# Kernel tuning notes

Measured on AMD Instinct MI355X. Metric: run time of the kernel, lower is better.

The kernel has to match this reference:

```python
import jax, jax.numpy as jnp
import numpy as np

B, H, W, C = 16, 64, 64, 256
NH = 8          # num_heads
WS = 8          # window size (8,8) from shift=2
HID = 1024      # mlp hidden = 4*C
EPS = 1e-5


def _rel_index():
    # relative_position_index exactly as in the torch module (meshgrid 'ij')
    ch = np.arange(WS)
    coords = np.stack(np.meshgrid(ch, ch, indexing='ij'))          # (2, WS, WS)
    flat = coords.reshape(2, -1)                                    # (2, N)
    rel = flat[:, :, None] - flat[:, None, :]                       # (2, N, N)
    rel = rel.transpose(1, 2, 0).astype(np.int64)                   # (N, N, 2)
    rel[..., 0] += WS - 1
    rel[..., 1] += WS - 1
    rel[..., 0] *= 2 * WS - 1
    return jnp.asarray(rel.sum(-1))                                 # (N, N)


def _ln(x, w, b):
    m = x.mean(-1, keepdims=True)
    v = jnp.mean((x - m) ** 2, axis=-1, keepdims=True)
    return (x - m) / jnp.sqrt(v + EPS) * w + b


def setup_inputs() -> dict:
    key = jax.random.key(0)
    ks = jax.random.split(key, 16)
    std = 0.02
    n_bias = (2 * WS - 1) * (2 * WS - 1)  # 225
    return {
        'x': jax.random.normal(ks[0], (B, H * W, C), jnp.float32),
        'norm1_w': jnp.ones((C,), jnp.float32),
        'norm1_b': jnp.zeros((C,), jnp.float32),
        'qkv_w': jax.random.normal(ks[1], (3 * C, C), jnp.float32) * std,
        'qkv_b': jnp.zeros((3 * C,), jnp.float32),
        'rel_bias': jax.random.normal(ks[2], (n_bias, NH), jnp.float32) * std,
        'proj_w': jax.random.normal(ks[3], (C, C), jnp.float32) * std,
        'proj_b': jnp.zeros((C,), jnp.float32),
        'norm2_w': jnp.ones((C,), jnp.float32),
        'norm2_b': jnp.zeros((C,), jnp.float32),
        'fc1_w': jax.random.normal(ks[4], (HID, C), jnp.float32) * std,
        'fc1_b': jnp.zeros((HID,), jnp.float32),
        'dw_w': jax.random.normal(ks[5], (3, 3, 1, HID), jnp.float32) * std,  # HWIO depthwise
        'dw_b': jnp.zeros((HID,), jnp.float32),
        'fc2_w': jax.random.normal(ks[6], (C, HID), jnp.float32) * std,
        'fc2_b': jnp.zeros((C,), jnp.float32),
    }


def reference(x, norm1_w, norm1_b, qkv_w, qkv_b, rel_bias, proj_w, proj_b,
              norm2_w, norm2_b, fc1_w, fc1_b, dw_w, dw_b, fc2_w, fc2_b):
    S = (H // WS) * (W // WS)   # num windows = 64
    N = WS * WS                 # tokens per window = 64
    shortcut = x
    h = _ln(x, norm1_w, norm1_b).reshape(B, H, W, C)
    # window partition -> (B, S, N, C), then permute to (B, N, S, C)
    hw = (h.reshape(B, H // WS, WS, W // WS, WS, C)
            .transpose(0, 1, 3, 2, 4, 5)
            .reshape(B, S, N, C))
    xw = hw.transpose(0, 2, 1, 3)            # (B, N, S, C)
    # qkv over flattened (N*S) tokens; heads split the S*C feature dim
    xf = xw.reshape(B, N * S, C)
    qkv = xf @ qkv_w.T + qkv_b               # (B, N*S, 3C)
    qkv = qkv.reshape(B, N, 3, NH, S * C // NH).transpose(2, 0, 3, 1, 4)
    q, k, v = qkv[0], qkv[1], qkv[2]         # (B, NH, N, S*C/NH)
    scale = (C // NH) ** -0.5
    attn = jnp.einsum('bhnd,bhmd->bhnm', q, k) * scale   # (B, NH, N, N)
    idx = _rel_index()
    bias = rel_bias[idx.reshape(-1)].reshape(N, N, NH).transpose(2, 0, 1)
    attn = jax.nn.softmax(attn + bias[None], axis=-1)
    out = jnp.einsum('bhnm,bhmd->bhnd', attn, v)         # (B, NH, N, S*C/NH)
    out = out.transpose(0, 2, 1, 3).reshape(B, N * S, C)
    out = (out @ proj_w.T + proj_b).reshape(B, N, S, C).transpose(0, 2, 1, 3)  # (B,S,N,C)
    # window reverse -> (B, H*W, C)
    xr = (out.reshape(B, H // WS, W // WS, WS, WS, C)
             .transpose(0, 1, 3, 2, 4, 5)
             .reshape(B, H * W, C))
    x = shortcut + xr
    # conv-based MLP (eval mode, dropout = identity)
    y = _ln(x, norm2_w, norm2_b).reshape(B, H, H, C)      # NHWC
    y = jnp.einsum('bhwc,oc->bhwo', y, fc1_w) + fc1_b     # 1x1 conv
    y = jax.lax.conv_general_dilated(
        y, dw_w, (1, 1), 'SAME',
        dimension_numbers=('NHWC', 'HWIO', 'NHWC'),
        feature_group_count=HID) + dw_b
    y = jax.nn.gelu(y, approximate=False)
    y = jnp.einsum('bhwo,co->bhwc', y, fc2_w) + fc2_b     # 1x1 conv
    return x + y.reshape(B, H * W, C)
```

## Files before the change

### kernel.cpp

```cpp
#include <hip/hip_runtime.h>
#include <hip/hip_bf16.h>
#include <cstdint>
#include <cstddef>

#define B_     16
#define HW_    4096
#define C_     256
#define NH_    8
#define S_     64
#define N_     64
#define C3_    768
#define HID_   1024
#define DHEAD_ 2048
#define EPS_   1e-5f

using u16 = unsigned short;
using u32 = unsigned int;

typedef __attribute__((ext_vector_type(8))) short bf16x8;
typedef __attribute__((ext_vector_type(4))) float f32x4;

__device__ __forceinline__ float bf2f(u16 u) {
  union { float f; u32 i; } x; x.i = ((u32)u) << 16; return x.f;
}
__device__ __forceinline__ u16 f2bf(float f) {
  union { float f; u32 i; } x; x.f = f;
  u32 r = (x.i + 0x7FFFu + ((x.i >> 16) & 1u)) >> 16;
  return (u16)r;
}

__device__ __forceinline__ void gload_lds16(const u16* g, u16* l) {
  __builtin_amdgcn_global_load_lds(
      (const __attribute__((address_space(1))) unsigned int*)g,
      (__attribute__((address_space(3))) unsigned int*)l, 16, 0, 0);
}

__launch_bounds__(256)
__global__ void f2bf_kernel(const float* __restrict__ in, u16* __restrict__ out) {
  int i = blockIdx.x * 256 + threadIdx.x;
  float4 v = ((const float4*)in)[i];
  ushort4 o = {f2bf(v.x), f2bf(v.y), f2bf(v.z), f2bf(v.w)};
  ((ushort4*)out)[i] = o;
}

__launch_bounds__(256)
__global__ void ln_kernel(const float* __restrict__ in, const float* __restrict__ w,
                          const float* __restrict__ bias, u16* __restrict__ out,
                          int b_base) {
  int wave = threadIdx.x >> 6;
  int lane = threadIdx.x & 63;
  int t = blockIdx.x * 4 + wave;
  int b = b_base + (t >> 12);
  int r = t & 4095;
  int n = r >> 6, s = r & 63;
  int hw = (((s >> 3) << 3) + (n >> 3)) * 64 + ((s & 7) << 3) + (n & 7);
  size_t src_row = ((size_t)b << 12) + hw;
  float4 v = ((const float4*)(in + src_row * C_))[lane];
  float sum = v.x + v.y + v.z + v.w;
#pragma unroll
  for (int off = 32; off; off >>= 1) sum += __shfl_xor(sum, off);
  float mean = sum * (1.0f / C_);
  float4 d = {v.x - mean, v.y - mean, v.z - mean, v.w - mean};
  float ss = d.x * d.x + d.y * d.y + d.z * d.z + d.w * d.w;
#pragma unroll
  for (int off = 32; off; off >>= 1) ss += __shfl_xor(ss, off);
  float rstd = rsqrtf(ss * (1.0f / C_) + EPS_);
  float4 w4 = ((const float4*)w)[lane];
  float4 b4 = ((const float4*)bias)[lane];
  ushort4 o;
  o.x = f2bf(d.x * rstd * w4.x + b4.x);
  o.y = f2bf(d.y * rstd * w4.y + b4.y);
  o.z = f2bf(d.z * rstd * w4.z + b4.z);
  o.w = f2bf(d.w * rstd * w4.w + b4.w);
  ((ushort4*)(out + (size_t)t * C_))[lane] = o;
}

template<int K_, int J_, int EPI>
__launch_bounds__(256)
__global__ void gemm_mfma(const u16* __restrict__ A, const u16* __restrict__ Wb,
                          const float* __restrict__ bias, u16* __restrict__ outB,
                          float* __restrict__ outF, const float* __restrict__ res,
                          int m_base, u16* __restrict__ qb, u16* __restrict__ kb,
                          u16* __restrict__ vt) {
  __shared__ u16 As[128 * 32];
  __shared__ u16 Bs[128 * 32];
  int tid = threadIdx.x;
  int wid = tid >> 6, lane = tid & 63;
  int n0 = blockIdx.x * 128;
  int m0 = blockIdx.y * 128;
  int wr = wid >> 1, wc = wid & 1;
  f32x4 acc[4][4] = {};

  int srow = lane >> 2;
  int scol = (lane & 3) * 8;

  for (int k0 = 0; k0 < K_; k0 += 32) {
#pragma unroll
    for (int r = 0; r < 2; ++r) {
      const u16* ga = A + (size_t)(m0 + r * 64 + wid * 16 + srow) * K_ + k0 + scol;
      gload_lds16(ga, &As[r * 2048 + wid * 512]);
      const u16* gb = Wb + (size_t)(n0 + r * 64 + wid * 16 + srow) * K_ + k0 + scol;
      gload_lds16(gb, &Bs[r * 2048 + wid * 512]);
    }
    __syncthreads();
    bf16x8 afr[4], bfr[4];
#pragma unroll
    for (int mf = 0; mf < 4; ++mf)
      afr[mf] = *(const bf16x8*)&As[(wr * 64 + mf * 16 + (lane & 15)) * 32 + (lane >> 4) * 8];
#pragma unroll
    for (int nf = 0; nf < 4; ++nf)
      bfr[nf] = *(const bf16x8*)&Bs[(wc * 64 + nf * 16 + (lane & 15)) * 32 + (lane >> 4) * 8];
#pragma unroll
    for (int mf = 0; mf < 4; ++mf)
#pragma unroll
      for (int nf = 0; nf < 4; ++nf)
        acc[mf][nf] = __builtin_amdgcn_mfma_f32_16x16x32_bf16(afr[mf], bfr[nf], acc[mf][nf], 0, 0, 0);
    __syncthreads();
  }

#pragma unroll
  for (int nf = 0; nf < 4; ++nf) {
    int col = n0 + wc * 64 + nf * 16 + (lane & 15);
    float bv = bias[col];
#pragma unroll
    for (int mf = 0; mf < 4; ++mf) {
#pragma unroll
      for (int j = 0; j < 4; ++j) {
        int m = m0 + wr * 64 + mf * 16 + (lane >> 4) * 4 + j;
        float v = acc[mf][nf][j] + bv;
        if (EPI == 0) {
          outB[(size_t)m * J_ + col] = f2bf(v);
        } else if (EPI == 2) {
          size_t o = (size_t)(m_base + m) * C_ + col;
          outF[o] += v;
        } else {
          int b_rel = m >> 12, nn = (m >> 6) & 63, s = m & 63;
          int f = s * 768 + col;
          int part = f >> 14, hh = (f >> 11) & 7, d = f & 2047;
          u16 val = f2bf(v);
          size_t bh = (size_t)b_rel * 8 + hh;
          if (part == 0)      qb[(bh * 64 + nn) * 2048 + d] = val;
          else if (part == 1) kb[(bh * 64 + nn) * 2048 + d] = val;
          else                vt[(bh * 2048 + d) * 64 + nn] = val;
        }
      }
    }
  }
}

__launch_bounds__(256)
__global__ void proj_ln_fused(const u16* __restrict__ A, const u16* __restrict__ Wb,
                              const float* __restrict__ bias, const float* __restrict__ res,
                              float* __restrict__ outF, const float* __restrict__ ln_w,
                              const float* __restrict__ ln_b, u16* __restrict__ h2,
                              int m_base) {
  __shared__ u16 As[64 * 32];
  __shared__ u16 Bs[256 * 32];
  __shared__ float red[64][8];
  int tid = threadIdx.x;
  int wid = tid >> 6, lane = tid & 63;
  int m0 = blockIdx.x * 64;
  f32x4 acc[4][4] = {};
  int srow = lane >> 2, scol = (lane & 3) * 8;

  for (int k0 = 0; k0 < 256; k0 += 32) {
    gload_lds16(A + (size_t)(m0 + wid * 16 + srow) * 256 + k0 + scol, &As[wid * 512]);
#pragma unroll
    for (int r = 0; r < 4; ++r)
      gload_lds16(Wb + (size_t)(r * 64 + wid * 16 + srow) * 256 + k0 + scol,
                  &Bs[(r * 64 + wid * 16) * 32]);
    __syncthreads();
    bf16x8 afr[4], bfr[4];
#pragma unroll
    for (int mf = 0; mf < 4; ++mf)
      afr[mf] = *(const bf16x8*)&As[(mf * 16 + (lane & 15)) * 32 + (lane >> 4) * 8];
#pragma unroll
    for (int nf = 0; nf < 4; ++nf)
      bfr[nf] = *(const bf16x8*)&Bs[(wid * 64 + nf * 16 + (lane & 15)) * 32 + (lane >> 4) * 8];
#pragma unroll
    for (int mf = 0; mf < 4; ++mf)
#pragma unroll
      for (int nf = 0; nf < 4; ++nf)
        acc[mf][nf] = __builtin_amdgcn_mfma_f32_16x16x32_bf16(afr[mf], bfr[nf], acc[mf][nf], 0, 0, 0);
    __syncthreads();
  }

#pragma unroll
  for (int mf = 0; mf < 4; ++mf) {
#pragma unroll
    for (int j = 0; j < 4; ++j) {
      int m = m0 + mf * 16 + (lane >> 4) * 4 + j;
      int gm = m_base + m;
      int b = gm >> 12, nn = (gm >> 6) & 63, s = gm & 63;
      int hw = (((s >> 3) << 3) + (nn >> 3)) * 64 + ((s & 7) << 3) + (nn & 7);
      size_t rowo = (((size_t)b << 12) + hw) * C_;
      float s1 = 0.f, s2 = 0.f;
#pragma unroll
      for (int nf = 0; nf < 4; ++nf) {
        int col = wid * 64 + nf * 16 + (lane & 15);
        float v = acc[mf][nf][j] + bias[col] + res[rowo + col];
        acc[mf][nf][j] = v;
        outF[rowo + col] = v;
        s1 += v; s2 += v * v;
      }
#pragma unroll
      for (int off = 1; off < 16; off <<= 1) {
        s1 += __shfl_xor(s1, off);
        s2 += __shfl_xor(s2, off);
      }
      if ((lane & 15) == 0) {
        int rr = mf * 16 + (lane >> 4) * 4 + j;
        red[rr][wid * 2] = s1;
        red[rr][wid * 2 + 1] = s2;
      }
    }
  }
  __syncthreads();

#pragma unroll
  for (int mf = 0; mf < 4; ++mf) {
#pragma unroll
    for (int j = 0; j < 4; ++j) {
      int rr = mf * 16 + (lane >> 4) * 4 + j;
      float sum = red[rr][0] + red[rr][2] + red[rr][4] + red[rr][6];
      float ssq = red[rr][1] + red[rr][3] + red[rr][5] + red[rr][7];
      float mean = sum * (1.0f / C_);
      float var = ssq * (1.0f / C_) - mean * mean;
      float rstd = rsqrtf(var + EPS_);
      int m = m0 + rr;
      int b_rel = m >> 12, nn = (m >> 6) & 63, s = m & 63;
      int hw = (((s >> 3) << 3) + (nn >> 3)) * 64 + ((s & 7) << 3) + (nn & 7);
      size_t ho = (((size_t)b_rel << 12) + hw) * C_;
#pragma unroll
      for (int nf = 0; nf < 4; ++nf) {
        int col = wid * 64 + nf * 16 + (lane & 15);
        float nv = (acc[mf][nf][j] - mean) * rstd * ln_w[col] + ln_b[col];
        h2[ho + col] = f2bf(nv);
      }
    }
  }
}

__launch_bounds__(256)
__global__ void attn_mfma(const u16* __restrict__ qb, const u16* __restrict__ kb,
                          const u16* __restrict__ vt, const float* __restrict__ rel_bias,
                          u16* __restrict__ outp) {
  __shared__ u16 bufA[4096];
  __shared__ u16 bufB[4096];
  int bh = blockIdx.x;
  int h = bh & 7;
  int b_rel = bh >> 3;
  int tid = threadIdx.x;
  int w = tid >> 6, lane = tid & 63;
  int l3 = lane >> 3, l7 = lane & 7;
  const u16* qg = qb + (size_t)bh * 64 * 2048;
  const u16* kg = kb + (size_t)bh * 64 * 2048;
  const u16* vg = vt + (size_t)bh * 2048 * 64;

  f32x4 acc[4] = {};
  for (int k0 = 0; k0 < 2048; k0 += 64) {
#pragma unroll
    for (int r = 0; r < 2; ++r) {
      int row = w * 16 + r * 8 + l3;
      int sc = (l7 ^ (row & 7)) * 8;
      gload_lds16(qg + (size_t)row * 2048 + k0 + sc, &bufA[(w * 16 + r * 8) * 64]);
      gload_lds16(kg + (size_t)row * 2048 + k0 + sc, &bufB[(w * 16 + r * 8) * 64]);
    }
    __syncthreads();
    int rowq = w * 16 + (lane & 15);
#pragma unroll
    for (int ks = 0; ks < 2; ++ks) {
      bf16x8 aq = *(const bf16x8*)&bufA[rowq * 64 + (((ks * 4 + (lane >> 4)) ^ (rowq & 7)) << 3)];
#pragma unroll
      for (int cf = 0; cf < 4; ++cf) {
        int m = cf * 16 + (lane & 15);
        bf16x8 bk = *(const bf16x8*)&bufB[m * 64 + (((ks * 4 + (lane >> 4)) ^ (m & 7)) << 3)];
        acc[cf] = __builtin_amdgcn_mfma_f32_16x16x32_bf16(aq, bk, acc[cf], 0, 0, 0);
      }
    }
    __syncthreads();
  }

  const float scale = 0.17677669529663688f;
#pragma unroll
  for (int j = 0; j < 4; ++j) {
    int r = w * 16 + (lane >> 4) * 4 + j;
    int i1 = r >> 3, j1 = r & 7;
    float v[4];
#pragma unroll
    for (int cf = 0; cf < 4; ++cf) {
      int c = cf * 16 + (lane & 15);
      int idx = (i1 - (c >> 3) + 7) * 15 + (j1 - (c & 7) + 7);
      v[cf] = acc[cf][j] * scale + rel_bias[idx * NH_ + h];
    }
    float mx = fmaxf(fmaxf(v[0], v[1]), fmaxf(v[2], v[3]));
#pragma unroll
    for (int off = 8; off; off >>= 1) mx = fmaxf(mx, __shfl_xor(mx, off));
    float sm = 0.f;
#pragma unroll
    for (int cf = 0; cf < 4; ++cf) { v[cf] = __expf(v[cf] - mx); sm += v[cf]; }
#pragma unroll
    for (int off = 8; off; off >>= 1) sm += __shfl_xor(sm, off);
    float inv = 1.0f / sm;
#pragma unroll
    for (int cf = 0; cf < 4; ++cf) {
      int c = cf * 16 + (lane & 15);
      bufA[r * 64 + (c ^ ((r & 7) << 3))] = f2bf(v[cf] * inv);
    }
  }
  __syncthreads();

  bf16x8 pa[2];
  {
    int n = w * 16 + (lane & 15);
#pragma unroll
    for (int ks = 0; ks < 2; ++ks)
      pa[ks] = *(const bf16x8*)&bufA[n * 64 + ((ks * 32 + (lane >> 4) * 8) ^ ((n & 7) << 3))];
  }

  for (int d0 = 0; d0 < 2048; d0 += 64) {
#pragma unroll
    for (int r = 0; r < 2; ++r) {
      int drow = w * 16 + r * 8 + l3;
      int sc = (l7 ^ (drow & 7)) * 8;
      gload_lds16(vg + (size_t)(d0 + drow) * 64 + sc, &bufB[(w * 16 + r * 8) * 64]);
    }
    __syncthreads();
    f32x4 o[4] = {};
#pragma unroll
    for (int ks = 0; ks < 2; ++ks)
#pragma unroll
      for (int cf = 0; cf < 4; ++cf) {
        int d = cf * 16 + (lane & 15);
        bf16x8 bv = *(const bf16x8*)&bufB[d * 64 + (((ks * 4 + (lane >> 4)) ^ (d & 7)) << 3)];
        o[cf] = __builtin_amdgcn_mfma_f32_16x16x32_bf16(pa[ks], bv, o[cf], 0, 0, 0);
      }
#pragma unroll
    for (int cf = 0; cf < 4; ++cf) {
      int f = h * 2048 + d0 + cf * 16 + (lane & 15);
      int s = f >> 8, c = f & 255;
#pragma unroll
      for (int j = 0; j < 4; ++j) {
        int n = w * 16 + (lane >> 4) * 4 + j;
        outp[(((size_t)b_rel * 64 + n) * 64 + s) * 256 + c] = f2bf(o[cf][j]);
      }
    }
    __syncthreads();
  }
}

__launch_bounds__(256)
__global__ void dwconv_gelu(const u16* __restrict__ y1, const float* __restrict__ dw_w,
                            const float* __restrict__ dw_b, u16* __restrict__ y2) {
  int bid = blockIdx.x;
  int wt = bid & 31, ht = (bid >> 5) & 15, b = bid >> 9;
  int h0 = ht * 4, w0 = wt * 2;
  int c0 = threadIdx.x * 4;

  float4 wv[9];
#pragma unroll
  for (int i = 0; i < 9; ++i) wv[i] = *(const float4*)&dw_w[i * HID_ + c0];

  ushort4 in[6][4];
#pragma unroll
  for (int ii = 0; ii < 6; ++ii) {
    int hh = h0 + ii - 1;
#pragma unroll
    for (int jj = 0; jj < 4; ++jj) {
      int ww = w0 + jj - 1;
      if ((unsigned)hh < 64u && (unsigned)ww < 64u)
        in[ii][jj] = *(const ushort4*)(y1 + ((size_t)((b << 12) + hh * 64 + ww)) * HID_ + c0);
      else
        in[ii][jj] = ushort4{0, 0, 0, 0};
    }
  }

  float4 bv = *(const float4*)&dw_b[c0];
  float4 acc[4][2];
#pragma unroll
  for (int i = 0; i < 4; ++i)
#pragma unroll
    for (int j = 0; j < 2; ++j) acc[i][j] = bv;

#pragma unroll
  for (int ii = 0; ii < 6; ++ii) {
#pragma unroll
    for (int jj = 0; jj < 4; ++jj) {
      ushort4 u = in[ii][jj];
      float4 f = {bf2f(u.x), bf2f(u.y), bf2f(u.z), bf2f(u.w)};
#pragma unroll
      for (int kh = 0; kh < 3; ++kh) {
        int i = ii - kh;
        if (i < 0 || i > 3) continue;
#pragma unroll
        for (int kw = 0; kw < 3; ++kw) {
          int j = jj - kw;
          if (j < 0 || j > 1) continue;
          float4 w4 = wv[kh * 3 + kw];
          acc[i][j].x += f.x * w4.x;
          acc[i][j].y += f.y * w4.y;
          acc[i][j].z += f.z * w4.z;
          acc[i][j].w += f.w * w4.w;
        }
      }
    }
  }

  const float k = 0.70710678118654752f;
#pragma unroll
  for (int i = 0; i < 4; ++i) {
#pragma unroll
    for (int j = 0; j < 2; ++j) {
      float4 a = acc[i][j];
      ushort4 o;
      o.x = f2bf(0.5f * a.x * (1.0f + erff(a.x * k)));
      o.y = f2bf(0.5f * a.y * (1.0f + erff(a.y * k)));
      o.z = f2bf(0.5f * a.z * (1.0f + erff(a.z * k)));
      o.w = f2bf(0.5f * a.w * (1.0f + erff(a.w * k)));
      *(ushort4*)(y2 + ((size_t)((b << 12) + (h0 + i) * 64 + (w0 + j))) * HID_ + c0) = o;
    }
  }
}

extern "C" void kernel_launch(void* const* d_in, const int* in_sizes, int n_in,
                              void* d_out, int out_size, void* d_ws, size_t ws_size,
                              hipStream_t stream) {
  const float* x       = (const float*)d_in[0];
  const float* norm1_w = (const float*)d_in[1];
  const float* norm1_b = (const float*)d_in[2];
  const float* qkv_w   = (const float*)d_in[3];
  const float* qkv_b   = (const float*)d_in[4];
  const float* rel_b   = (const float*)d_in[5];
  const float* proj_w  = (const float*)d_in[6];
  const float* proj_b  = (const float*)d_in[7];
  const float* norm2_w = (const float*)d_in[8];
  const float* norm2_b = (const float*)d_in[9];
  const float* fc1_w   = (const float*)d_in[10];
  const float* fc1_b   = (const float*)d_in[11];
  const float* dw_w    = (const float*)d_in[12];
  const float* dw_b    = (const float*)d_in[13];
  const float* fc2_w   = (const float*)d_in[14];
  const float* fc2_b   = (const float*)d_in[15];
  float* out = (float*)d_out;
  char* ws = (char*)d_ws;

  u16* wq = (u16*)(ws);
  u16* wp = wq + 768 * 256;
  u16* w1 = wp + 256 * 256;
  u16* w2 = w1 + 1024 * 256;
  f2bf_kernel<<<768 * 256 / 1024, 256, 0, stream>>>(qkv_w, wq);
  f2bf_kernel<<<256 * 256 / 1024, 256, 0, stream>>>(proj_w, wp);
  f2bf_kernel<<<1024 * 256 / 1024, 256, 0, stream>>>(fc1_w, w1);
  f2bf_kernel<<<1024 * 256 / 1024, 256, 0, stream>>>(fc2_w, w2);

  const size_t MBy = (size_t)1 << 20;
  char* cws = ws + 2 * MBy;
  int G = 1;
  for (int g = 16; g >= 1; g >>= 1) {
    if (2 * MBy + (size_t)(18 * g) * MBy <= ws_size) { G = g; break; }
  }
  const size_t gm = (size_t)G * MBy;
  u16* h1c    = (u16*)(cws);
  u16* qbuf   = (u16*)(cws + 2 * gm);
  u16* kbuf   = (u16*)(cws + 4 * gm);
  u16* vtbuf  = (u16*)(cws + 6 * gm);
  u16* attnoc = (u16*)(cws + 8 * gm);
  u16* h2c    = (u16*)(cws);
  u16* y1c    = (u16*)(cws + 2 * gm);
  u16* y2c    = (u16*)(cws + 10 * gm);

  const int Mloc = G * 4096;
  for (int b0 = 0; b0 < B_; b0 += G) {
    ln_kernel<<<Mloc / 4, 256, 0, stream>>>(x, norm1_w, norm1_b, h1c, b0);
    gemm_mfma<256, 768, 3><<<dim3(6, Mloc / 128), 256, 0, stream>>>(
        h1c, wq, qkv_b, nullptr, nullptr, nullptr, 0, qbuf, kbuf, vtbuf);
    attn_mfma<<<G * 8, 256, 0, stream>>>(qbuf, kbuf, vtbuf, rel_b, attnoc);
    proj_ln_fused<<<Mloc / 64, 256, 0, stream>>>(
        attnoc, wp, proj_b, x, out, norm2_w, norm2_b, h2c, b0 * 4096);
    gemm_mfma<256, 1024, 0><<<dim3(8, Mloc / 128), 256, 0, stream>>>(
        h2c, w1, fc1_b, y1c, nullptr, nullptr, 0, nullptr, nullptr, nullptr);
    dwconv_gelu<<<Mloc / 8, 256, 0, stream>>>(y1c, dw_w, dw_b, y2c);
    gemm_mfma<1024, 256, 2><<<dim3(2, Mloc / 128), 256, 0, stream>>>(
        y2c, w2, fc2_b, nullptr, out, nullptr, b0 * 4096, nullptr, nullptr, nullptr);
  }
}
```

Measured before the change: 533.6 us.

## Widen GEMM K-tile to 128 with XOR-swizzled LDS layout

Both MFMA GEMM kernels now stage 128-wide K slices per iteration instead of 32, and run four inner MFMA sub-steps per barrier pair. LDS rows are XOR-swizzled by row index to avoid bank conflicts on the bf16x8 fragment reads. Launch bounds now request 2 blocks per CU. This cuts barrier and loop overhead per unit of work, at the cost of much larger LDS use (64KB in gemm, ~82KB in proj_ln), which may limit occupancy and leaves loads unpipelined.

```diff
diff --git a/kernel.cpp b/kernel.cpp
--- a/kernel.cpp
+++ b/kernel.cpp
@@ -76,14 +76,14 @@
 }
 
 template<int K_, int J_, int EPI>
-__launch_bounds__(256)
+__launch_bounds__(256, 2)
 __global__ void gemm_mfma(const u16* __restrict__ A, const u16* __restrict__ Wb,
                           const float* __restrict__ bias, u16* __restrict__ outB,
                           float* __restrict__ outF, const float* __restrict__ res,
                           int m_base, u16* __restrict__ qb, u16* __restrict__ kb,
                           u16* __restrict__ vt) {
-  __shared__ u16 As[128 * 32];
-  __shared__ u16 Bs[128 * 32];
+  __shared__ u16 As[128 * 128];
+  __shared__ u16 Bs[128 * 128];
   int tid = threadIdx.x;
   int wid = tid >> 6, lane = tid & 63;
   int n0 = blockIdx.x * 128;
@@ -91,30 +91,41 @@
   int wr = wid >> 1, wc = wid & 1;
   f32x4 acc[4][4] = {};
 
-  int srow = lane >> 2;
-  int scol = (lane & 3) * 8;
-
-  for (int k0 = 0; k0 < K_; k0 += 32) {
-#pragma unroll
-    for (int r = 0; r < 2; ++r) {
-      const u16* ga = A + (size_t)(m0 + r * 64 + wid * 16 + srow) * K_ + k0 + scol;
-      gload_lds16(ga, &As[r * 2048 + wid * 512]);
-      const u16* gb = Wb + (size_t)(n0 + r * 64 + wid * 16 + srow) * K_ + k0 + scol;
-      gload_lds16(gb, &Bs[r * 2048 + wid * 512]);
-    }
-    __syncthreads();
-    bf16x8 afr[4], bfr[4];
-#pragma unroll
-    for (int mf = 0; mf < 4; ++mf)
-      afr[mf] = *(const bf16x8*)&As[(wr * 64 + mf * 16 + (lane & 15)) * 32 + (lane >> 4) * 8];
-#pragma unroll
-    for (int nf = 0; nf < 4; ++nf)
-      bfr[nf] = *(const bf16x8*)&Bs[(wc * 64 + nf * 16 + (lane & 15)) * 32 + (lane >> 4) * 8];
-#pragma unroll
-    for (int mf = 0; mf < 4; ++mf)
-#pragma unroll
-      for (int nf = 0; nf < 4; ++nf)
-        acc[mf][nf] = __builtin_amdgcn_mfma_f32_16x16x32_bf16(afr[mf], bfr[nf], acc[mf][nf], 0, 0, 0);
+  int l16r = lane >> 4;
+  int l16c = lane & 15;
+
+  for (int k0 = 0; k0 < K_; k0 += 128) {
+#pragma unroll
+    for (int r = 0; r < 8; ++r) {
+      int lrow = wid * 32 + r * 4 + l16r;
+      int cb = (l16c * 16) ^ ((lrow & 7) << 4);
+      gload_lds16(A + (size_t)(m0 + lrow) * K_ + k0 + (cb >> 1),
+                  &As[(wid * 32 + r * 4) * 128]);
+      gload_lds16(Wb + (size_t)(n0 + lrow) * K_ + k0 + (cb >> 1),
+                  &Bs[(wid * 32 + r * 4) * 128]);
+    }
+    __syncthreads();
+#pragma unroll
+    for (int kk = 0; kk < 4; ++kk) {
+      bf16x8 afr[4], bfr[4];
+#pragma unroll
+      for (int mf = 0; mf < 4; ++mf) {
+        int ra = wr * 64 + mf * 16 + l16c;
+        int cb = (kk * 64 + l16r * 16) ^ ((ra & 7) << 4);
+        afr[mf] = *(const bf16x8*)&As[ra * 128 + (cb >> 1)];
+      }
+#pragma unroll
+      for (int nf = 0; nf < 4; ++nf) {
+        int rb = wc * 64 + nf * 16 + l16c;
+        int cb = (kk * 64 + l16r * 16) ^ ((rb & 7) << 4);
+        bfr[nf] = *(const bf16x8*)&Bs[rb * 128 + (cb >> 1)];
+      }
+#pragma unroll
+      for (int mf = 0; mf < 4; ++mf)
+#pragma unroll
+        for (int nf = 0; nf < 4; ++nf)
+          acc[mf][nf] = __builtin_amdgcn_mfma_f32_16x16x32_bf16(afr[mf], bfr[nf], acc[mf][nf], 0, 0, 0);
+    }
     __syncthreads();
   }
 
@@ -148,40 +159,58 @@
   }
 }
 
-__launch_bounds__(256)
+__launch_bounds__(256, 2)
 __global__ void proj_ln_fused(const u16* __restrict__ A, const u16* __restrict__ Wb,
                               const float* __restrict__ bias, const float* __restrict__ res,
                               float* __restrict__ outF, const float* __restrict__ ln_w,
                               const float* __restrict__ ln_b, u16* __restrict__ h2,
                               int m_base) {
-  __shared__ u16 As[64 * 32];
-  __shared__ u16 Bs[256 * 32];
+  __shared__ u16 As[64 * 128];
+  __shared__ u16 Bs[256 * 128];
   __shared__ float red[64][8];
   int tid = threadIdx.x;
   int wid = tid >> 6, lane = tid & 63;
   int m0 = blockIdx.x * 64;
   f32x4 acc[4][4] = {};
-  int srow = lane >> 2, scol = (lane & 3) * 8;
-
-  for (int k0 = 0; k0 < 256; k0 += 32) {
-    gload_lds16(A + (size_t)(m0 + wid * 16 + srow) * 256 + k0 + scol, &As[wid * 512]);
-#pragma unroll
-    for (int r = 0; r < 4; ++r)
-      gload_lds16(Wb + (size_t)(r * 64 + wid * 16 + srow) * 256 + k0 + scol,
-                  &Bs[(r * 64 + wid * 16) * 32]);
-    __syncthreads();
-    bf16x8 afr[4], bfr[4];
-#pragma unroll
-    for (int mf = 0; mf < 4; ++mf)
-      afr[mf] = *(const bf16x8*)&As[(mf * 16 + (lane & 15)) * 32 + (lane >> 4) * 8];
-#pragma unroll
-    for (int nf = 0; nf < 4; ++nf)
-      bfr[nf] = *(const bf16x8*)&Bs[(wid * 64 + nf * 16 + (lane & 15)) * 32 + (lane >> 4) * 8];
-#pragma unroll
-    for (int mf = 0; mf < 4; ++mf)
-#pragma unroll
-      for (int nf = 0; nf < 4; ++nf)
-        acc[mf][nf] = __builtin_amdgcn_mfma_f32_16x16x32_bf16(afr[mf], bfr[nf], acc[mf][nf], 0, 0, 0);
+  int l16r = lane >> 4, l16c = lane & 15;
+
+  for (int k0 = 0; k0 < 256; k0 += 128) {
+#pragma unroll
+    for (int r = 0; r < 4; ++r) {
+      int lrow = wid * 16 + r * 4 + l16r;
+      int cb = (l16c * 16) ^ ((lrow & 7) << 4);
+      gload_lds16(A + (size_t)(m0 + lrow) * 256 + k0 + (cb >> 1),
+                  &As[(wid * 16 + r * 4) * 128]);
+    }
+#pragma unroll
+    for (int r = 0; r < 16; ++r) {
+      int lrow = wid * 64 + r * 4 + l16r;
+      int cb = (l16c * 16) ^ ((lrow & 7) << 4);
+      gload_lds16(Wb + (size_t)lrow * 256 + k0 + (cb >> 1),
+                  &Bs[(wid * 64 + r * 4) * 128]);
+    }
+    __syncthreads();
+#pragma unroll
+    for (int kk = 0; kk < 4; ++kk) {
+      bf16x8 afr[4], bfr[4];
+#pragma unroll
+      for (int mf = 0; mf < 4; ++mf) {
+        int ra = mf * 16 + l16c;
+        int cb = (kk * 64 + l16r * 16) ^ ((ra & 7) << 4);
+        afr[mf] = *(const bf16x8*)&As[ra * 128 + (cb >> 1)];
+      }
+#pragma unroll
+      for (int nf = 0; nf < 4; ++nf) {
+        int rb = wid * 64 + nf * 16 + l16c;
+        int cb = (kk * 64 + l16r * 16) ^ ((rb & 7) << 4);
+        bfr[nf] = *(const bf16x8*)&Bs[rb * 128 + (cb >> 1)];
+      }
+#pragma unroll
+      for (int mf = 0; mf < 4; ++mf)
+#pragma unroll
+        for (int nf = 0; nf < 4; ++nf)
+          acc[mf][nf] = __builtin_amdgcn_mfma_f32_16x16x32_bf16(afr[mf], bfr[nf], acc[mf][nf], 0, 0, 0);
+    }
     __syncthreads();
   }
 
```

New measurement: 547.1 us. 2.5% more time.

## Pack weights into MFMA fragment order and load GEMM operands directly from global

Applied to the files above, without the earlier changes.

Weight conversion kernels now write bf16 weights pre-permuted into per-lane MFMA fragment order. The GEMM and proj+LN kernels drop their LDS staging and barriers and load both A and B fragments straight from global memory into registers. This removes LDS traffic and __syncthreads. In exchange, A rows are now read redundantly by different waves, the loads are strided, and nothing overlaps them with the MFMAs.

```diff
diff --git a/kernel.cpp b/kernel.cpp
--- a/kernel.cpp
+++ b/kernel.cpp
@@ -36,11 +36,23 @@
 }
 
 __launch_bounds__(256)
-__global__ void f2bf_kernel(const float* __restrict__ in, u16* __restrict__ out) {
-  int i = blockIdx.x * 256 + threadIdx.x;
-  float4 v = ((const float4*)in)[i];
-  ushort4 o = {f2bf(v.x), f2bf(v.y), f2bf(v.z), f2bf(v.w)};
-  ((ushort4*)out)[i] = o;
+__global__ void pack_w_kernel(const float* __restrict__ W, u16* __restrict__ out,
+                              int K, int kshift) {
+  int g = blockIdx.x * 256 + threadIdx.x;
+  int lane = g & 63;
+  int pk = g >> 6;
+  int cb = pk >> kshift;
+  int kb = pk & ((1 << kshift) - 1);
+  int j = cb * 16 + (lane & 15);
+  int k = kb * 32 + ((lane >> 4) << 3);
+  const float* src = W + (size_t)j * K + k;
+  float4 a = ((const float4*)src)[0];
+  float4 b = ((const float4*)src)[1];
+  ushort4 lo = {f2bf(a.x), f2bf(a.y), f2bf(a.z), f2bf(a.w)};
+  ushort4 hi = {f2bf(b.x), f2bf(b.y), f2bf(b.z), f2bf(b.w)};
+  ushort4* dst = (ushort4*)(out + (size_t)g * 8);
+  dst[0] = lo;
+  dst[1] = hi;
 }
 
 __launch_bounds__(256)
@@ -77,13 +89,12 @@
 
 template<int K_, int J_, int EPI>
 __launch_bounds__(256)
-__global__ void gemm_mfma(const u16* __restrict__ A, const u16* __restrict__ Wb,
+__global__ void gemm_mfma(const u16* __restrict__ A, const u16* __restrict__ wpk,
                           const float* __restrict__ bias, u16* __restrict__ outB,
                           float* __restrict__ outF, const float* __restrict__ res,
                           int m_base, u16* __restrict__ qb, u16* __restrict__ kb,
                           u16* __restrict__ vt) {
-  __shared__ u16 As[128 * 32];
-  __shared__ u16 Bs[128 * 32];
+  constexpr int NKB = K_ / 32;
   int tid = threadIdx.x;
   int wid = tid >> 6, lane = tid & 63;
   int n0 = blockIdx.x * 128;
@@ -91,31 +102,26 @@
   int wr = wid >> 1, wc = wid & 1;
   f32x4 acc[4][4] = {};
 
-  int srow = lane >> 2;
-  int scol = (lane & 3) * 8;
-
-  for (int k0 = 0; k0 < K_; k0 += 32) {
-#pragma unroll
-    for (int r = 0; r < 2; ++r) {
-      const u16* ga = A + (size_t)(m0 + r * 64 + wid * 16 + srow) * K_ + k0 + scol;
-      gload_lds16(ga, &As[r * 2048 + wid * 512]);
-      const u16* gb = Wb + (size_t)(n0 + r * 64 + wid * 16 + srow) * K_ + k0 + scol;
-      gload_lds16(gb, &Bs[r * 2048 + wid * 512]);
-    }
-    __syncthreads();
+  const u16* arow[4];
+#pragma unroll
+  for (int mf = 0; mf < 4; ++mf)
+    arow[mf] = A + (size_t)(m0 + wr * 64 + mf * 16 + (lane & 15)) * K_ + ((lane >> 4) << 3);
+  const u16* bbase = wpk + ((size_t)((n0 >> 4) + wc * 4) * NKB * 64 + lane) * 8;
+
+#pragma unroll
+  for (int kb32 = 0; kb32 < NKB; ++kb32) {
     bf16x8 afr[4], bfr[4];
 #pragma unroll
     for (int mf = 0; mf < 4; ++mf)
-      afr[mf] = *(const bf16x8*)&As[(wr * 64 + mf * 16 + (lane & 15)) * 32 + (lane >> 4) * 8];
+      afr[mf] = *(const bf16x8*)(arow[mf] + kb32 * 32);
 #pragma unroll
     for (int nf = 0; nf < 4; ++nf)
-      bfr[nf] = *(const bf16x8*)&Bs[(wc * 64 + nf * 16 + (lane & 15)) * 32 + (lane >> 4) * 8];
+      bfr[nf] = *(const bf16x8*)(bbase + ((size_t)nf * NKB + kb32) * 64 * 8);
 #pragma unroll
     for (int mf = 0; mf < 4; ++mf)
 #pragma unroll
       for (int nf = 0; nf < 4; ++nf)
         acc[mf][nf] = __builtin_amdgcn_mfma_f32_16x16x32_bf16(afr[mf], bfr[nf], acc[mf][nf], 0, 0, 0);
-    __syncthreads();
   }
 
 #pragma unroll
@@ -149,40 +155,37 @@
 }
 
 __launch_bounds__(256)
-__global__ void proj_ln_fused(const u16* __restrict__ A, const u16* __restrict__ Wb,
+__global__ void proj_ln_fused(const u16* __restrict__ A, const u16* __restrict__ wpk,
                               const float* __restrict__ bias, const float* __restrict__ res,
                               float* __restrict__ outF, const float* __restrict__ ln_w,
                               const float* __restrict__ ln_b, u16* __restrict__ h2,
                               int m_base) {
-  __shared__ u16 As[64 * 32];
-  __shared__ u16 Bs[256 * 32];
   __shared__ float red[64][8];
   int tid = threadIdx.x;
   int wid = tid >> 6, lane = tid & 63;
   int m0 = blockIdx.x * 64;
   f32x4 acc[4][4] = {};
-  int srow = lane >> 2, scol = (lane & 3) * 8;
-
-  for (int k0 = 0; k0 < 256; k0 += 32) {
-    gload_lds16(A + (size_t)(m0 + wid * 16 + srow) * 256 + k0 + scol, &As[wid * 512]);
-#pragma unroll
-    for (int r = 0; r < 4; ++r)
-      gload_lds16(Wb + (size_t)(r * 64 + wid * 16 + srow) * 256 + k0 + scol,
-                  &Bs[(r * 64 + wid * 16) * 32]);
-    __syncthreads();
+
+  const u16* arow[4];
+#pragma unroll
+  for (int mf = 0; mf < 4; ++mf)
+    arow[mf] = A + (size_t)(m0 + mf * 16 + (lane & 15)) * 256 + ((lane >> 4) << 3);
+  const u16* bbase = wpk + ((size_t)(wid * 4) * 8 * 64 + lane) * 8;
+
+#pragma unroll
+  for (int kb32 = 0; kb32 < 8; ++kb32) {
     bf16x8 afr[4], bfr[4];
 #pragma unroll
     for (int mf = 0; mf < 4; ++mf)
-      afr[mf] = *(const bf16x8*)&As[(mf * 16 + (lane & 15)) * 32 + (lane >> 4) * 8];
+      afr[mf] = *(const bf16x8*)(arow[mf] + kb32 * 32);
 #pragma unroll
     for (int nf = 0; nf < 4; ++nf)
-      bfr[nf] = *(const bf16x8*)&Bs[(wid * 64 + nf * 16 + (lane & 15)) * 32 + (lane >> 4) * 8];
+      bfr[nf] = *(const bf16x8*)(bbase + ((size_t)nf * 8 + kb32) * 64 * 8);
 #pragma unroll
     for (int mf = 0; mf < 4; ++mf)
 #pragma unroll
       for (int nf = 0; nf < 4; ++nf)
         acc[mf][nf] = __builtin_amdgcn_mfma_f32_16x16x32_bf16(afr[mf], bfr[nf], acc[mf][nf], 0, 0, 0);
-    __syncthreads();
   }
 
 #pragma unroll
@@ -448,10 +451,10 @@
   u16* wp = wq + 768 * 256;
   u16* w1 = wp + 256 * 256;
   u16* w2 = w1 + 1024 * 256;
-  f2bf_kernel<<<768 * 256 / 1024, 256, 0, stream>>>(qkv_w, wq);
-  f2bf_kernel<<<256 * 256 / 1024, 256, 0, stream>>>(proj_w, wp);
-  f2bf_kernel<<<1024 * 256 / 1024, 256, 0, stream>>>(fc1_w, w1);
-  f2bf_kernel<<<1024 * 256 / 1024, 256, 0, stream>>>(fc2_w, w2);
+  pack_w_kernel<<<768 * 256 / 8 / 256, 256, 0, stream>>>(qkv_w, wq, 256, 3);
+  pack_w_kernel<<<256 * 256 / 8 / 256, 256, 0, stream>>>(proj_w, wp, 256, 3);
+  pack_w_kernel<<<1024 * 256 / 8 / 256, 256, 0, stream>>>(fc1_w, w1, 256, 3);
+  pack_w_kernel<<<256 * 1024 / 8 / 256, 256, 0, stream>>>(fc2_w, w2, 1024, 5);
 
   const size_t MBy = (size_t)1 << 20;
   char* cws = ws + 2 * MBy;
```

Result: slower. 625.4 us (+17.2%).
